# Kernel tuning notes

Hardware: AMD Instinct MI355X
Metric: run time of the kernel (lower is better)

The kernel has to match this reference:

```python
import jax, jax.numpy as jnp
import numpy as np

V, BLK, L, H, E = 50257, 1024, 12, 12, 768
HS = E // H
B = 2


def _ln(x, w, b, eps=1e-5):
    mu = jnp.mean(x, axis=-1, keepdims=True)
    var = jnp.mean((x - mu) ** 2, axis=-1, keepdims=True)
    return (x - mu) * jax.lax.rsqrt(var + eps) * w + b


def setup_inputs() -> dict:
    key = jax.random.key(0)
    ks = jax.random.split(key, 16)
    s = 0.02
    inp = {
        "x": jax.random.randint(ks[0], (B, BLK), 0, V),
        "tok_emb": jax.random.normal(ks[1], (V, E), jnp.float32) * s,
        "pos_emb": jax.random.normal(ks[2], (BLK, E), jnp.float32) * s,
        "qW": jax.random.normal(ks[3], (L, H, HS, E), jnp.float32) * s,
        "kW": jax.random.normal(ks[4], (L, H, HS, E), jnp.float32) * s,
        "vW": jax.random.normal(ks[5], (L, H, HS, E), jnp.float32) * s,
        "ln1_w": jnp.ones((L, E), jnp.float32),
        "ln1_b": jnp.zeros((L, E), jnp.float32),
        "fc1_w": jax.random.normal(ks[6], (L, 4 * E, E), jnp.float32) * s,
        "fc1_b": jnp.zeros((L, 4 * E), jnp.float32),
        "fc2_w": jax.random.normal(ks[7], (L, E, 4 * E), jnp.float32) * s,
        "fc2_b": jnp.zeros((L, E), jnp.float32),
        "ln2_w": jnp.ones((L, E), jnp.float32),
        "ln2_b": jnp.zeros((L, E), jnp.float32),
        "lnf_w": jnp.ones((E,), jnp.float32),
        "lnf_b": jnp.zeros((E,), jnp.float32),
        "lm_w": jax.random.normal(ks[8], (V, E), jnp.float32) * s,
    }
    return inp


def _gpt(x, tok_emb, pos_emb, qW, kW, vW, ln1_w, ln1_b, fc1_w, fc1_b,
         fc2_w, fc2_b, ln2_w, ln2_b, lnf_w, lnf_b, lm_w):
    T = x.shape[1]
    h = tok_emb[x] + pos_emb[None, :T]  # [B,T,E]
    scale = 1.0 / jnp.sqrt(jnp.asarray(E, h.dtype))  # C**0.5 with C=n_embd
    causal = jnp.tril(jnp.ones((T, T), bool))  # mask where tril==0
    for l in range(L):
        q = jnp.einsum("bte,hde->bthd", h, qW[l])
        k = jnp.einsum("bte,hde->bthd", h, kW[l])
        v = jnp.einsum("bte,hde->bthd", h, vW[l])
        # faithful to source: w = k @ q^T / sqrt(n_embd); rows index k, cols index q
        w = jnp.einsum("bshd,bthd->bhst", k, q) * scale
        w = jnp.where(causal[None, None], w, -jnp.inf)
        w = jax.nn.softmax(w, axis=-1)
        a = jnp.einsum("bhst,bthd->bshd", w, v)  # [B,T,H,HS]
        a = a.reshape(a.shape[0], T, E)  # head-major concat
        h = _ln(h + a, ln1_w[l], ln1_b[l])
        m = jax.nn.gelu(jnp.einsum("bte,fe->btf", h, fc1_w[l]) + fc1_b[l],
                        approximate=False)
        m = jnp.einsum("btf,ef->bte", m, fc2_w[l]) + fc2_b[l]
        h = _ln(h + m, ln2_w[l], ln2_b[l])
    h = _ln(h, lnf_w, lnf_b)
    return jnp.einsum("bte,ve->btv", h, lm_w)


def reference(x, tok_emb, pos_emb, qW, kW, vW, ln1_w, ln1_b, fc1_w, fc1_b,
              fc2_w, fc2_b, ln2_w, ln2_b, lnf_w, lnf_b, lm_w):
    return _gpt(x, tok_emb, pos_emb, qW, kW, vW, ln1_w, ln1_b, fc1_w, fc1_b,
                fc2_w, fc2_b, ln2_w, ln2_b, lnf_w, lnf_b, lm_w)
```

## Files before the change

### kernel.cpp

```cpp
#include <hip/hip_runtime.h>
#include <math.h>

typedef unsigned short u16;
typedef __attribute__((ext_vector_type(8))) short short8;
typedef __attribute__((ext_vector_type(8))) u16 ushort8_t;
typedef __attribute__((ext_vector_type(4))) u16 ushort4_t;
typedef __attribute__((ext_vector_type(4))) float f32x4;

#define BB 2
#define TT 1024
#define EE 768
#define HH 12
#define HSZ 64
#define LL 12
#define FF 3072
#define VV 50257
#define VPAD 50304
#define MM 2048
#define NQKV 2304
#define QKW 1536
#define KVB 128
#define BK 64

__device__ __forceinline__ float bf2f(u16 u) {
    union { unsigned int i; float f; } c;
    c.i = ((unsigned int)u) << 16;
    return c.f;
}
__device__ __forceinline__ u16 f2bf(float f) {
    unsigned int u = __float_as_uint(f);
    unsigned int r = (u + 0x7FFFu + ((u >> 16) & 1u)) >> 16;
    return (u16)r;
}

__device__ __forceinline__ void gload_lds16(const void* g, void* l) {
    __builtin_amdgcn_global_load_lds(
        (const __attribute__((address_space(1))) unsigned int*)g,
        (__attribute__((address_space(3))) unsigned int*)l,
        16, 0, 0);
}

template<int N> __device__ __forceinline__ void waitcnt_vm() {
    if      constexpr (N == 0)  asm volatile("s_waitcnt vmcnt(0)" ::: "memory");
    else if constexpr (N == 4)  asm volatile("s_waitcnt vmcnt(4)" ::: "memory");
    else if constexpr (N == 6)  asm volatile("s_waitcnt vmcnt(6)" ::: "memory");
    else if constexpr (N == 8)  asm volatile("s_waitcnt vmcnt(8)" ::: "memory");
    else if constexpr (N == 12) asm volatile("s_waitcnt vmcnt(12)" ::: "memory");
    else static_assert(N == 0, "unsupported vmcnt");
}

__device__ __forceinline__ void xcd_swizzle(int& bx, int& by) {
    int nx = gridDim.x;
    int nwg = nx * gridDim.y;
    int orig = blockIdx.x + blockIdx.y * nx;
    int q = nwg >> 3, r = nwg & 7;
    int xcd = orig & 7, idx = orig >> 3;
    int nf = (xcd < r ? xcd * (q + 1) : r * (q + 1) + (xcd - r) * q) + idx;
    bx = nf % nx;
    by = nf / nx;
}

__global__ __launch_bounds__(256)
void cast_all_kernel(const float* __restrict__ qW, const float* __restrict__ kW,
                     const float* __restrict__ vW, const float* __restrict__ fc1w,
                     const float* __restrict__ fc2w, const float* __restrict__ lmw,
                     u16* __restrict__ wqkv, u16* __restrict__ wfc1,
                     u16* __restrict__ wfc2, u16* __restrict__ wlm)
{
    const int j = blockIdx.y;
    const float* s;
    u16* d;
    long total, per, stride;
    switch (j) {
    case 0: s = qW;   d = wqkv;              total = (long)LL * EE * EE; per = (long)EE * EE; stride = (long)NQKV * EE; break;
    case 1: s = kW;   d = wqkv + EE * EE;     total = (long)LL * EE * EE; per = (long)EE * EE; stride = (long)NQKV * EE; break;
    case 2: s = vW;   d = wqkv + 2 * EE * EE; total = (long)LL * EE * EE; per = (long)EE * EE; stride = (long)NQKV * EE; break;
    case 3: s = fc1w; d = wfc1;              total = (long)LL * FF * EE; per = total; stride = total; break;
    case 4: s = fc2w; d = wfc2;              total = (long)LL * EE * FF; per = total; stride = total; break;
    default: s = lmw; d = wlm;               total = (long)VV * EE;      per = total; stride = total; break;
    }
    long step = (long)gridDim.x * blockDim.x * 4;
    for (long i = ((long)blockIdx.x * blockDim.x + threadIdx.x) * 4; i < total; i += step) {
        long layer = i / per;
        long off = i - layer * per;
        float4 v = *reinterpret_cast<const float4*>(s + i);
        ushort4_t o;
        o[0] = f2bf(v.x); o[1] = f2bf(v.y); o[2] = f2bf(v.z); o[3] = f2bf(v.w);
        *reinterpret_cast<ushort4_t*>(d + layer * stride + off) = o;
    }
}

__global__ void embed_kernel(const int* __restrict__ x, const float* __restrict__ tok,
                             const float* __restrict__ pos, float* __restrict__ h,
                             u16* __restrict__ hb)
{
    int row = blockIdx.x;
    int t = row & (TT - 1);
    int id = x[row];
    const float* tr = tok + (size_t)id * EE;
    const float* pr = pos + (size_t)t * EE;
    for (int i = threadIdx.x; i < EE; i += blockDim.x) {
        float v = tr[i] + pr[i];
        h[(size_t)row * EE + i] = v;
        hb[(size_t)row * EE + i] = f2bf(v);
    }
}

__global__ __launch_bounds__(256)
void add_ln_kernel(const float* __restrict__ hin, const float* __restrict__ add,
                   const float* __restrict__ w, const float* __restrict__ bias,
                   float* __restrict__ hout, u16* __restrict__ hbout)
{
    int lane = threadIdx.x & 63, wv = threadIdx.x >> 6;
    int row = blockIdx.x * 4 + wv;
    const float* hp = hin + (size_t)row * EE;
    float x[12];
    float s = 0.f;
#pragma unroll
    for (int c = 0; c < 3; ++c) {
        float4 hv = *reinterpret_cast<const float4*>(hp + c * 256 + lane * 4);
        if (add) {
            float4 av = *reinterpret_cast<const float4*>(add + (size_t)row * EE + c * 256 + lane * 4);
            hv.x += av.x; hv.y += av.y; hv.z += av.z; hv.w += av.w;
        }
        x[c * 4 + 0] = hv.x; x[c * 4 + 1] = hv.y; x[c * 4 + 2] = hv.z; x[c * 4 + 3] = hv.w;
        s += hv.x + hv.y + hv.z + hv.w;
    }
#pragma unroll
    for (int o = 32; o > 0; o >>= 1) s += __shfl_xor(s, o);
    float mu = s * (1.0f / EE);
    float vs = 0.f;
#pragma unroll
    for (int i = 0; i < 12; ++i) { float d = x[i] - mu; vs += d * d; }
#pragma unroll
    for (int o = 32; o > 0; o >>= 1) vs += __shfl_xor(vs, o);
    float inv = 1.0f / sqrtf(vs * (1.0f / EE) + 1e-5f);
#pragma unroll
    for (int c = 0; c < 3; ++c) {
        int col = c * 256 + lane * 4;
        float4 wv4 = *reinterpret_cast<const float4*>(w + col);
        float4 bv4 = *reinterpret_cast<const float4*>(bias + col);
        float4 o;
        o.x = (x[c * 4 + 0] - mu) * inv * wv4.x + bv4.x;
        o.y = (x[c * 4 + 1] - mu) * inv * wv4.y + bv4.y;
        o.z = (x[c * 4 + 2] - mu) * inv * wv4.z + bv4.z;
        o.w = (x[c * 4 + 3] - mu) * inv * wv4.w + bv4.w;
        *reinterpret_cast<float4*>(hout + (size_t)row * EE + col) = o;
        ushort4_t ob;
        ob[0] = f2bf(o.x); ob[1] = f2bf(o.y); ob[2] = f2bf(o.z); ob[3] = f2bf(o.w);
        *reinterpret_cast<ushort4_t*>(hbout + (size_t)row * EE + col) = ob;
    }
}

enum { EPI_GELU_BF16 = 1, EPI_BIAS_F32 = 2, EPI_F32 = 3, EPI_QKV = 4 };

template<int EPI, bool NGUARD, int DEPTH, int MR, int NR>
__global__ __launch_bounds__(256, 2)
void gemm_kernel(const u16* __restrict__ A, const u16* __restrict__ Bw,
                 const float* __restrict__ bias, void* __restrict__ Cout,
                 void* __restrict__ vTout, int Ndim, int Kdim)
{
    constexpr int BMT = MR * 32;
    constexpr int BNT = NR * 32;
    constexpr int NLD = MR + NR;
    __shared__ u16 As[DEPTH * BMT * BK];
    __shared__ u16 Bs[DEPTH * BNT * BK];
    const int tid = threadIdx.x;
    const int lane = tid & 63;
    const int wid = tid >> 6;
    const int wm = wid >> 1, wn = wid & 1;
    int bx, by;
    xcd_swizzle(bx, by);
    const int rowBase = bx * BMT;
    const int colBase = by * BNT;

    const int srow = lane >> 3;
    const int scol = ((lane & 7) ^ srow) * 8;

#define GSTAGE(k0_, buf_)                                                         \
    {                                                                             \
        _Pragma("unroll")                                                         \
        for (int i_ = 0; i_ < MR; ++i_) {                                         \
            int r0_ = (wid * MR + i_) * 8;                                        \
            gload_lds16(A + (size_t)(rowBase + r0_ + srow) * Kdim + (k0_) + scol, \
                        As + (buf_) * (BMT * BK) + r0_ * BK);                     \
        }                                                                         \
        _Pragma("unroll")                                                         \
        for (int i_ = 0; i_ < NR; ++i_) {                                         \
            int r0_ = (wid * NR + i_) * 8;                                        \
            gload_lds16(Bw + (size_t)(colBase + r0_ + srow) * Kdim + (k0_) + scol,\
                        Bs + (buf_) * (BNT * BK) + r0_ * BK);                     \
        }                                                                         \
    }

#define COMPUTE(Asb_, Bsb_)                                                       \
    {                                                                             \
        const int fr = lane & 15;                                                 \
        const int qd = lane >> 4;                                                 \
        _Pragma("unroll")                                                         \
        for (int kk = 0; kk < 2; ++kk) {                                          \
            short8 af[MR], bfr[NR];                                               \
            int goff = (((kk * 4 + qd) ^ (fr & 7))) * 8;                          \
            _Pragma("unroll")                                                     \
            for (int mi = 0; mi < MR; ++mi)                                       \
                af[mi] = *reinterpret_cast<const short8*>(                        \
                    &(Asb_)[(wm * (MR * 16) + mi * 16 + fr) * BK + goff]);        \
            _Pragma("unroll")                                                     \
            for (int ni = 0; ni < NR; ++ni)                                       \
                bfr[ni] = *reinterpret_cast<const short8*>(                       \
                    &(Bsb_)[(wn * (NR * 16) + ni * 16 + fr) * BK + goff]);        \
            _Pragma("unroll")                                                     \
            for (int mi = 0; mi < MR; ++mi)                                       \
                _Pragma("unroll")                                                 \
                for (int ni = 0; ni < NR; ++ni)                                   \
                    acc[mi][ni] = __builtin_amdgcn_mfma_f32_16x16x32_bf16(        \
                        af[mi], bfr[ni], acc[mi][ni], 0, 0, 0);                   \
        }                                                                         \
    }

    f32x4 acc[MR][NR] = {};
    const int nk = Kdim / BK;

    if (DEPTH > 1) {
#pragma unroll
        for (int p = 0; p < DEPTH; ++p) GSTAGE(p * BK, p)
        int cur = 0;
        for (int t = 0; t < nk; ++t) {
            int rem = nk - 1 - t;
            if (rem >= DEPTH - 1)            waitcnt_vm<NLD * (DEPTH - 1)>();
            else if (DEPTH > 2 && rem == 1)  waitcnt_vm<NLD>();
            else                             waitcnt_vm<0>();
            __builtin_amdgcn_s_barrier();
            const u16* Asb = As + cur * (BMT * BK);
            const u16* Bsb = Bs + cur * (BNT * BK);
            COMPUTE(Asb, Bsb)
            __builtin_amdgcn_s_barrier();
            if (t + DEPTH < nk) GSTAGE((t + DEPTH) * BK, cur)
            cur = (cur + 1 == DEPTH) ? 0 : cur + 1;
        }
    } else {
        for (int t = 0; t < nk; ++t) {
            GSTAGE(t * BK, 0)
            __syncthreads();
            COMPUTE(As, Bs)
            __syncthreads();
        }
    }

    if (EPI == EPI_QKV && colBase >= QKW) {
        u16* T = Bs;
        __syncthreads();
#pragma unroll
        for (int mi = 0; mi < MR; ++mi)
#pragma unroll
            for (int ni = 0; ni < NR; ++ni)
#pragma unroll
                for (int r = 0; r < 4; ++r) {
                    int lr = wm * (MR * 16) + mi * 16 + (lane >> 4) * 4 + r;
                    int lc = wn * (NR * 16) + ni * 16 + (lane & 15);
                    T[lc * 72 + lr] = f2bf(acc[mi][ni][r]);
                }
        __syncthreads();
        constexpr int SEGS = BMT / 32;
        int hdl = tid / SEGS;
        int seg = (tid % SEGS) * 32;
        if (hdl < BNT) {
            int b_ = rowBase >> 10;
            int t0 = rowBase & (TT - 1);
            u16* dst = (u16*)vTout + ((size_t)b_ * EE + (colBase - QKW) + hdl) * TT + t0 + seg;
            const u16* src = T + hdl * 72 + seg;
#pragma unroll
            for (int j = 0; j < 4; ++j)
                *reinterpret_cast<ushort8_t*>(dst + j * 8) =
                    *reinterpret_cast<const ushort8_t*>(src + j * 8);
        }
        return;
    }

#pragma unroll
    for (int mi = 0; mi < MR; ++mi) {
#pragma unroll
        for (int ni = 0; ni < NR; ++ni) {
#pragma unroll
            for (int r = 0; r < 4; ++r) {
                int row = rowBase + wm * (MR * 16) + mi * 16 + (lane >> 4) * 4 + r;
                int col = colBase + wn * (NR * 16) + ni * 16 + (lane & 15);
                if (NGUARD && col >= Ndim) continue;
                float v = acc[mi][ni][r];
                if (EPI == EPI_GELU_BF16) { v += bias[col]; v = 0.5f * v * (1.0f + erff(v * 0.70710678f)); }
                if (EPI == EPI_BIAS_F32)  { v += bias[col]; }
                size_t idx = (size_t)row * Ndim + col;
                if (EPI == EPI_QKV) {
                    ((u16*)Cout)[(size_t)row * QKW + col] = f2bf(v);
                } else if (EPI == EPI_GELU_BF16) {
                    ((u16*)Cout)[idx] = f2bf(v);
                } else {
                    ((float*)Cout)[idx] = v;
                }
            }
        }
    }
}

__global__ __launch_bounds__(256)
void attn_kernel(const u16* __restrict__ qkb, const u16* __restrict__ vT,
                 float* __restrict__ aout)
{
    __shared__ u16 Qs[2 * KVB * 64];
    __shared__ u16 Vs[2 * 64 * KVB];
    __shared__ u16 Ps[4 * 16 * KVB];

    const int lane = threadIdx.x & 63;
    const int wv = threadIdx.x >> 6;
    int bxs, bys;
    xcd_swizzle(bxs, bys);
    const int js = (gridDim.x - 1) - bxs;
    const int s0 = js * 64;
    const int smax = s0 + 63;
    const int bh = bys;
    const int b = bh / HH, h = bh % HH;
    const int bT = b * TT;
    const float scale = 0.036084392f;

    short8 af[2];
    {
        int srow = bT + s0 + wv * 16 + (lane & 15);
#pragma unroll
        for (int kk = 0; kk < 2; ++kk)
            af[kk] = *reinterpret_cast<const short8*>(
                qkb + (size_t)srow * QKW + EE + h * HSZ + kk * 32 + (lane >> 4) * 8);
    }

    const int ntiles = (s0 + 63) / KVB + 1;
    const int qrow = lane >> 3;
    const int qu = lane & 7;
    const int vrow = lane >> 4;
    const int vu = lane & 15;

#define ASTAGE(jt2_, buf_)                                                            \
    {                                                                                 \
        int tb_ = (jt2_) * KVB;                                                       \
        _Pragma("unroll")                                                             \
        for (int i_ = 0; i_ < 4; ++i_) {                                              \
            int R0_ = wv * 32 + i_ * 8;                                               \
            int row_ = R0_ + qrow;                                                    \
            gload_lds16(qkb + (size_t)(bT + tb_ + row_) * QKW + h * HSZ               \
                            + ((qu ^ (row_ & 7)) * 8),                                \
                        &Qs[(buf_) * (KVB * 64) + R0_ * 64]);                         \
        }                                                                             \
        _Pragma("unroll")                                                             \
        for (int i_ = 0; i_ < 4; ++i_) {                                              \
            int R0_ = wv * 16 + i_ * 4;                                               \
            int row_ = R0_ + vrow;                                                    \
            gload_lds16(vT + ((size_t)b * EE + h * HSZ + row_) * TT + tb_             \
                            + ((vu ^ (row_ & 15)) * 8),                               \
                        &Vs[(buf_) * (64 * KVB) + R0_ * KVB]);                        \
        }                                                                             \
    }

    ASTAGE(0, 0)

    float m[4], l[4];
    f32x4 oacc[4] = {};
#pragma unroll
    for (int r = 0; r < 4; ++r) { m[r] = -INFINITY; l[r] = 0.f; }

    int cur = 0;
    for (int jt2 = 0; jt2 < ntiles; ++jt2) {
        __syncthreads();
        if (jt2 + 1 < ntiles) ASTAGE(jt2 + 1, cur ^ 1)

        const u16* Qb = &Qs[cur * (KVB * 64)];
        const u16* Vb = &Vs[cur * (64 * KVB)];
        const int tb = jt2 * KVB;
        const int navail = smax - tb;
        const int nact = min(8, (navail >> 4) + 1);
        const int nkc  = min(4, (navail >> 5) + 1);
        const bool dg = (tb + KVB - 1 > s0);

        f32x4 sc[8];
#pragma unroll
        for (int ni = 0; ni < 8; ++ni) {
            if (ni < nact) {
                f32x4 a = {};
                int trow = ni * 16 + (lane & 15);
#pragma unroll
                for (int kk = 0; kk < 2; ++kk) {
                    int g = kk * 4 + (lane >> 4);
                    short8 bq = *reinterpret_cast<const short8*>(
                        &Qb[trow * 64 + ((g ^ (trow & 7)) * 8)]);
                    a = __builtin_amdgcn_mfma_f32_16x16x32_bf16(af[kk], bq, a, 0, 0, 0);
                }
                sc[ni] = a;
            } else {
                f32x4 mn = {-1e30f, -1e30f, -1e30f, -1e30f};
                sc[ni] = mn;
            }
        }

        if (dg) {
#pragma unroll
            for (int ni = 0; ni < 8; ++ni)
#pragma unroll
                for (int r = 0; r < 4; ++r) {
                    float sv = sc[ni][r] * scale;
                    int t = tb + ni * 16 + (lane & 15);
                    int s = s0 + wv * 16 + (lane >> 4) * 4 + r;
                    if (t > s) sv = -1e30f;
                    sc[ni][r] = sv;
                }
        } else {
#pragma unroll
            for (int ni = 0; ni < 8; ++ni)
#pragma unroll
                for (int r = 0; r < 4; ++r) sc[ni][r] *= scale;
        }

        f32x4 pexp[8];
#pragma unroll
        for (int r = 0; r < 4; ++r) {
            float rm = sc[0][r];
#pragma unroll
            for (int ni = 1; ni < 8; ++ni) rm = fmaxf(rm, sc[ni][r]);
#pragma unroll
            for (int o = 1; o < 16; o <<= 1) rm = fmaxf(rm, __shfl_xor(rm, o));
            float mnew = fmaxf(m[r], rm);
            float alpha = __expf(m[r] - mnew);
            m[r] = mnew;
            float rs = 0.f;
#pragma unroll
            for (int ni = 0; ni < 8; ++ni) {
                float p;
                if (ni < nact) p = __expf(sc[ni][r] - mnew);
                else p = 0.f;
                pexp[ni][r] = p;
                rs += p;
            }
#pragma unroll
            for (int o = 1; o < 16; o <<= 1) rs += __shfl_xor(rs, o);
            l[r] = l[r] * alpha + rs;
#pragma unroll
            for (int dt = 0; dt < 4; ++dt) oacc[dt][r] *= alpha;
        }

        const int nst = nkc * 2;
#pragma unroll
        for (int ni = 0; ni < 8; ++ni) {
            if (ni < nst) {
#pragma unroll
                for (int r = 0; r < 4; ++r) {
                    int sl = (lane >> 4) * 4 + r;
                    int tl = ni * 16 + (lane & 15);
                    Ps[wv * (16 * KVB) + sl * KVB + (((tl >> 3) ^ sl) & 15) * 8 + (tl & 7)]
                        = f2bf(pexp[ni][r]);
                }
            }
        }

#pragma unroll
        for (int kc = 0; kc < 4; ++kc) {
            if (kc < nkc) {
                int srow = lane & 15;
                int g = kc * 4 + (lane >> 4);
                short8 pa = *reinterpret_cast<const short8*>(
                    &Ps[wv * (16 * KVB) + srow * KVB + ((g ^ srow) & 15) * 8]);
#pragma unroll
                for (int dt = 0; dt < 4; ++dt) {
                    int drow = dt * 16 + (lane & 15);
                    short8 bv = *reinterpret_cast<const short8*>(
                        &Vb[drow * KVB + (((kc * 4 + (lane >> 4)) ^ drow) & 15) * 8]);
                    oacc[dt] = __builtin_amdgcn_mfma_f32_16x16x32_bf16(pa, bv, oacc[dt], 0, 0, 0);
                }
            }
        }
        cur ^= 1;
    }

    float invl[4];
#pragma unroll
    for (int r = 0; r < 4; ++r) invl[r] = 1.0f / l[r];
#pragma unroll
    for (int dt = 0; dt < 4; ++dt)
#pragma unroll
        for (int r = 0; r < 4; ++r) {
            int sg = s0 + wv * 16 + (lane >> 4) * 4 + r;
            aout[(size_t)(bT + sg) * EE + h * HSZ + dt * 16 + (lane & 15)] =
                oacc[dt][r] * invl[r];
        }
}

extern "C" void kernel_launch(void* const* d_in, const int* in_sizes, int n_in,
                              void* d_out, int out_size, void* d_ws, size_t ws_size,
                              hipStream_t stream)
{
    const int*   x    = (const int*)d_in[0];
    const float* tok  = (const float*)d_in[1];
    const float* pos  = (const float*)d_in[2];
    const float* qW   = (const float*)d_in[3];
    const float* kW   = (const float*)d_in[4];
    const float* vW   = (const float*)d_in[5];
    const float* ln1w = (const float*)d_in[6];
    const float* ln1b = (const float*)d_in[7];
    const float* fc1w = (const float*)d_in[8];
    const float* fc1b = (const float*)d_in[9];
    const float* fc2w = (const float*)d_in[10];
    const float* fc2b = (const float*)d_in[11];
    const float* ln2w = (const float*)d_in[12];
    const float* ln2b = (const float*)d_in[13];
    const float* lnfw = (const float*)d_in[14];
    const float* lnfb = (const float*)d_in[15];
    const float* lmw  = (const float*)d_in[16];
    float* out = (float*)d_out;

    char* ws = (char*)d_ws;
    u16* wqkv = (u16*)ws;  ws += (size_t)LL * NQKV * EE * 2;
    u16* wfc1 = (u16*)ws;  ws += (size_t)LL * FF * EE * 2;
    u16* wfc2 = (u16*)ws;  ws += (size_t)LL * EE * FF * 2;
    u16* wlm  = (u16*)ws;  ws += (size_t)VPAD * EE * 2;
    float* h    = (float*)ws; ws += (size_t)MM * EE * 4;
    float* tmp  = (float*)ws; ws += (size_t)MM * EE * 4;
    u16* qkb = (u16*)ws;      ws += (size_t)MM * QKW * 2;
    u16* vTb = (u16*)ws;      ws += (size_t)BB * EE * TT * 2;
    u16* hb  = (u16*)ws;      ws += (size_t)MM * EE * 2;
    u16* mb  = (u16*)ws;      ws += (size_t)MM * FF * 2;

    dim3 blk(256);

    cast_all_kernel<<<dim3(1024, 6), blk, 0, stream>>>(
        qW, kW, vW, fc1w, fc2w, lmw, wqkv, wfc1, wfc2, wlm);

    embed_kernel<<<MM, blk, 0, stream>>>(x, tok, pos, h, hb);

    dim3 gQKV(MM / 64, NQKV / 128);
    dim3 gF1(MM / 64, FF / 128);
    dim3 gF2(MM / 64, EE / 64);
    dim3 gV(MM / 64, VPAD / 128);
    dim3 gAttn(TT / 64, BB * HH);

    for (int l = 0; l < LL; ++l) {
        gemm_kernel<EPI_QKV, false, 2, 2, 4><<<gQKV, blk, 0, stream>>>(
            hb, wqkv + (size_t)l * NQKV * EE, nullptr, qkb, vTb, NQKV, EE);
        attn_kernel<<<gAttn, blk, 0, stream>>>(qkb, vTb, tmp);
        add_ln_kernel<<<MM / 4, blk, 0, stream>>>(h, tmp, ln1w + l * EE, ln1b + l * EE, h, hb);
        gemm_kernel<EPI_GELU_BF16, false, 2, 2, 4><<<gF1, blk, 0, stream>>>(
            hb, wfc1 + (size_t)l * FF * EE, fc1b + (size_t)l * FF, mb, nullptr, FF, EE);
        gemm_kernel<EPI_BIAS_F32, false, 3, 2, 2><<<gF2, blk, 0, stream>>>(
            mb, wfc2 + (size_t)l * EE * FF, fc2b + (size_t)l * EE, tmp, nullptr, EE, FF);
        add_ln_kernel<<<MM / 4, blk, 0, stream>>>(h, tmp, ln2w + l * EE, ln2b + l * EE, h, hb);
    }
    add_ln_kernel<<<MM / 4, blk, 0, stream>>>(h, nullptr, lnfw, lnfb, h, hb);
    gemm_kernel<EPI_F32, true, 2, 2, 4><<<gV, blk, 0, stream>>>(
        hb, wlm, nullptr, out, nullptr, VV, EE);
}
```

Baseline: 2.020 ms.

## Generalize GEMM warp layout and use 256x128 tiles with 8 waves for LM head

Templates the GEMM kernel on a warp grid (WM x WN) so the tile size and thread count are no longer fixed at 4 waves. The existing layers keep their old tile geometry. The vocab projection now uses 256x128 tiles with 512 threads, single-buffered LDS and 4x4 MFMA fragments per wave. This raises operand reuse on the largest GEMM and cuts redundant loads of the lm weight. The costs are losing double buffering, higher register pressure, and fewer blocks (8 row tiles) competing for the CUs.

Result: faster. 1.958 ms (-3.1%).

```diff
diff --git a/kernel.cpp b/kernel.cpp
--- a/kernel.cpp
+++ b/kernel.cpp
@@ -154,21 +154,25 @@
 
 enum { EPI_GELU_BF16 = 1, EPI_BIAS_F32 = 2, EPI_F32 = 3, EPI_QKV = 4 };
 
-template<int EPI, bool NGUARD, int DEPTH, int MR, int NR>
-__global__ __launch_bounds__(256, 2)
+template<int EPI, bool NGUARD, int DEPTH, int WM, int WN, int MR, int NR>
+__global__ __launch_bounds__(WM * WN * 64, 2)
 void gemm_kernel(const u16* __restrict__ A, const u16* __restrict__ Bw,
                  const float* __restrict__ bias, void* __restrict__ Cout,
                  void* __restrict__ vTout, int Ndim, int Kdim)
 {
-    constexpr int BMT = MR * 32;
-    constexpr int BNT = NR * 32;
-    constexpr int NLD = MR + NR;
+    constexpr int NW  = WM * WN;
+    constexpr int BMT = WM * MR * 16;
+    constexpr int BNT = WN * NR * 16;
+    constexpr int CA  = BMT / (8 * NW);
+    constexpr int CB  = BNT / (8 * NW);
+    constexpr int NLD = CA + CB;
+    static_assert(BMT % (8 * NW) == 0 && BNT % (8 * NW) == 0, "stage geom");
     __shared__ u16 As[DEPTH * BMT * BK];
     __shared__ u16 Bs[DEPTH * BNT * BK];
     const int tid = threadIdx.x;
     const int lane = tid & 63;
     const int wid = tid >> 6;
-    const int wm = wid >> 1, wn = wid & 1;
+    const int wm = wid / WN, wn = wid % WN;
     int bx, by;
     xcd_swizzle(bx, by);
     const int rowBase = bx * BMT;
@@ -180,14 +184,14 @@
 #define GSTAGE(k0_, buf_)                                                         \
     {                                                                             \
         _Pragma("unroll")                                                         \
-        for (int i_ = 0; i_ < MR; ++i_) {                                         \
-            int r0_ = (wid * MR + i_) * 8;                                        \
+        for (int i_ = 0; i_ < CA; ++i_) {                                         \
+            int r0_ = (wid * CA + i_) * 8;                                        \
             gload_lds16(A + (size_t)(rowBase + r0_ + srow) * Kdim + (k0_) + scol, \
                         As + (buf_) * (BMT * BK) + r0_ * BK);                     \
         }                                                                         \
         _Pragma("unroll")                                                         \
-        for (int i_ = 0; i_ < NR; ++i_) {                                         \
-            int r0_ = (wid * NR + i_) * 8;                                        \
+        for (int i_ = 0; i_ < CB; ++i_) {                                         \
+            int r0_ = (wid * CB + i_) * 8;                                        \
             gload_lds16(Bw + (size_t)(colBase + r0_ + srow) * Kdim + (k0_) + scol,\
                         Bs + (buf_) * (BNT * BK) + r0_ * BK);                     \
         }                                                                         \
@@ -534,21 +538,21 @@
     dim3 gQKV(MM / 64, NQKV / 128);
     dim3 gF1(MM / 64, FF / 128);
     dim3 gF2(MM / 64, EE / 64);
-    dim3 gV(MM / 64, VPAD / 128);
+    dim3 gV(MM / 256, VPAD / 128);
     dim3 gAttn(TT / 64, BB * HH);
 
     for (int l = 0; l < LL; ++l) {
-        gemm_kernel<EPI_QKV, false, 2, 2, 4><<<gQKV, blk, 0, stream>>>(
+        gemm_kernel<EPI_QKV, false, 2, 2, 2, 2, 4><<<gQKV, blk, 0, stream>>>(
             hb, wqkv + (size_t)l * NQKV * EE, nullptr, qkb, vTb, NQKV, EE);
         attn_kernel<<<gAttn, blk, 0, stream>>>(qkb, vTb, tmp);
         add_ln_kernel<<<MM / 4, blk, 0, stream>>>(h, tmp, ln1w + l * EE, ln1b + l * EE, h, hb);
-        gemm_kernel<EPI_GELU_BF16, false, 2, 2, 4><<<gF1, blk, 0, stream>>>(
+        gemm_kernel<EPI_GELU_BF16, false, 2, 2, 2, 2, 4><<<gF1, blk, 0, stream>>>(
             hb, wfc1 + (size_t)l * FF * EE, fc1b + (size_t)l * FF, mb, nullptr, FF, EE);
-        gemm_kernel<EPI_BIAS_F32, false, 3, 2, 2><<<gF2, blk, 0, stream>>>(
+        gemm_kernel<EPI_BIAS_F32, false, 3, 2, 2, 2, 2><<<gF2, blk, 0, stream>>>(
             mb, wfc2 + (size_t)l * EE * FF, fc2b + (size_t)l * EE, tmp, nullptr, EE, FF);
         add_ln_kernel<<<MM / 4, blk, 0, stream>>>(h, tmp, ln2w + l * EE, ln2b + l * EE, h, hb);
     }
     add_ln_kernel<<<MM / 4, blk, 0, stream>>>(h, nullptr, lnfw, lnfb, h, hb);
-    gemm_kernel<EPI_F32, true, 2, 2, 4><<<gV, blk, 0, stream>>>(
+    gemm_kernel<EPI_F32, true, 1, 4, 2, 4, 4><<<gV, dim3(512), 0, stream>>>(
         hb, wlm, nullptr, out, nullptr, VV, EE);
 }
```
